# Kernel optimization log

Measured on AMD Instinct MI355X. Metric: run time of the kernel, lower is better.

## Reference

```python
import jax, jax.numpy as jnp
import numpy as np

B, N, D, H, K, R = 128, 2048, 256, 16, 32, 16
LEAKY_SLOPE = 0.01


def setup_inputs() -> dict:
    key = jax.random.key(0)
    ks = jax.random.split(key, 8)
    s = 0.05
    inp = jax.random.normal(ks[0], (B * N, D), dtype=jnp.float32)
    batch_ids = jnp.repeat(jnp.arange(B, dtype=jnp.int32), N)  # equal-size graphs
    Wk = jax.random.normal(ks[1], (K, D), dtype=jnp.float32) * s
    Wq0 = jax.random.normal(ks[2], (H * K, D), dtype=jnp.float32) * s
    Wq1 = jax.random.normal(ks[3], (H * K, D), dtype=jnp.float32) * s
    We = jax.random.normal(ks[4], (R, D), dtype=jnp.float32) * s
    Wout = jax.random.normal(ks[5], (D, H * R), dtype=jnp.float32) * s
    bout = jax.random.normal(ks[6], (D,), dtype=jnp.float32) * s
    return {"inp": inp, "batch_ids": batch_ids, "Wk": Wk, "Wq0": Wq0,
            "Wq1": Wq1, "We": We, "Wout": Wout, "bout": bout}


def reference(inp, batch_ids, Wk, Wq0, Wq1, We, Wout, bout):
    b = int(jnp.max(batch_ids)) + 1  # number of graphs (static at trace time)
    d = inp.shape[-1]
    # global max pool per graph (torch_geometric global_max_pool)
    pooled = jax.ops.segment_max(inp, batch_ids, num_segments=b)  # [B, D]
    x = inp.reshape(b, -1, d)                                     # [B, N, D]
    keys = jnp.einsum('bnd,kd->bnk', x, Wk)                       # [B, N, K]

    def head_embed(Wq):
        q = (pooled @ Wq.T).reshape(b, H, K)                      # [B, H, K]
        logits = jnp.einsum('bhk,bnk->bhn', q, keys)              # [B, H, N]
        att = jax.nn.softmax(logits, axis=-1)
        feat = jnp.einsum('bhn,bnd->bhd', att, x)                 # [B, H, D]
        return jnp.einsum('bhd,rd->bhr', feat, We)                # [B, H, R]

    dx = (head_embed(Wq0) - head_embed(Wq1)).reshape(b, -1)       # [B, H*R]
    out = dx @ Wout.T + bout
    return jnp.where(out >= 0, out, LEAKY_SLOPE * out)            # LeakyReLU
```

## Files before the change

### kernel.cpp

```cpp
#include <hip/hip_runtime.h>
#include <math.h>

#define B_ 128
#define N_ 2048
#define D_ 256
#define NHEADS 32

#define POOLED_OFF 0
#define PHI_OFF    32768
#define PLO_OFF    557056
#define ML_OFF     1081344
#define FEATP_OFF  1114112
#define XHI_OFF    5308416
#define XLO_OFF    38862848

#define XHI_S 0
#define XLO_S 32768
#define ATT_S 0
#define XT_S  33280
#define STAT_S 53760

typedef __attribute__((ext_vector_type(8))) short short8;
typedef __attribute__((ext_vector_type(4))) float f32x4;

__device__ __forceinline__ void atomic_max_f32(float* addr, float v) {
    if (v >= 0.0f) atomicMax((int*)addr, __float_as_int(v + 0.0f));
    else           atomicMin((unsigned int*)addr, __float_as_uint(v));
}
__device__ __forceinline__ unsigned short f2bf(float f) {
    unsigned u = __float_as_uint(f);
    u += 0x7fff + ((u >> 16) & 1);
    return (unsigned short)(u >> 16);
}
__device__ __forceinline__ float bf2f(unsigned short h) {
    return __uint_as_float(((unsigned)h) << 16);
}
__device__ __forceinline__ unsigned pack2bf(float a, float b) {
    return (unsigned)f2bf(a) | ((unsigned)f2bf(b) << 16);
}

__global__ __launch_bounds__(256) void k_init(float* __restrict__ pooled) {
    pooled[blockIdx.x * 256 + threadIdx.x] = -INFINITY;
}

__global__ __launch_bounds__(256) void k_pool(const float* __restrict__ inp,
                                              float* __restrict__ pooled,
                                              unsigned short* __restrict__ xhi,
                                              unsigned short* __restrict__ xlo) {
    int b = blockIdx.x >> 4;
    int ch = blockIdx.x & 15;
    int t = threadIdx.x;
    int sub = t >> 6;
    int dq = (t & 63) * 4;
    const float* p = inp + ((size_t)(b * N_ + ch * 128 + sub)) * D_ + dq;
    size_t nodebase = (size_t)b * N_ + ch * 128 + sub;
    float4 m = {-INFINITY, -INFINITY, -INFINITY, -INFINITY};
#pragma unroll 4
    for (int i = 0; i < 32; ++i) {
        float4 v = *(const float4*)(p + (size_t)i * 4 * D_);
        m.x = fmaxf(m.x, v.x); m.y = fmaxf(m.y, v.y);
        m.z = fmaxf(m.z, v.z); m.w = fmaxf(m.w, v.w);
        size_t node = nodebase + (size_t)i * 4;
        ushort4 h4, l4;
        h4.x = f2bf(v.x); l4.x = f2bf(v.x - bf2f(h4.x));
        h4.y = f2bf(v.y); l4.y = f2bf(v.y - bf2f(h4.y));
        h4.z = f2bf(v.z); l4.z = f2bf(v.z - bf2f(h4.z));
        h4.w = f2bf(v.w); l4.w = f2bf(v.w - bf2f(h4.w));
        *(ushort4*)(xhi + node * D_ + dq) = h4;
        *(ushort4*)(xlo + node * D_ + dq) = l4;
    }
    __shared__ float sm[4 * 256];
    sm[sub * 256 + dq + 0] = m.x;
    sm[sub * 256 + dq + 1] = m.y;
    sm[sub * 256 + dq + 2] = m.z;
    sm[sub * 256 + dq + 3] = m.w;
    __syncthreads();
    float v = fmaxf(fmaxf(sm[t], sm[256 + t]), fmaxf(sm[512 + t], sm[768 + t]));
    atomic_max_f32(pooled + b * D_ + t, v);
}

__global__ __launch_bounds__(256) void k_qp(const float* __restrict__ pooled,
                                            const float* __restrict__ Wq0,
                                            const float* __restrict__ Wq1,
                                            const float* __restrict__ Wk,
                                            unsigned short* __restrict__ Phi,
                                            unsigned short* __restrict__ Plo) {
    __shared__ float pl[D_];
    __shared__ float ql[1024];
    int b = blockIdx.x, t = threadIdx.x;
    pl[t] = pooled[b * D_ + t];
    __syncthreads();
    for (int rep = 0; rep < 4; ++rep) {
        int idx = rep * 256 + t;
        const float* Wq = (idx < 512) ? Wq0 : Wq1;
        int row = idx & 511;
        const float4* wr = (const float4*)(Wq + (size_t)row * D_);
        float acc = 0.0f;
        for (int dqi = 0; dqi < 64; ++dqi) {
            float4 w = wr[dqi];
            const float* pp = &pl[dqi * 4];
            acc += w.x * pp[0] + w.y * pp[1] + w.z * pp[2] + w.w * pp[3];
        }
        ql[idx] = acc;
    }
    __syncthreads();
    float wk[32];
#pragma unroll
    for (int k = 0; k < 32; ++k) wk[k] = Wk[k * D_ + t];
    for (int j = 0; j < NHEADS; ++j) {
        const float* q = &ql[(j >> 4) * 512 + (j & 15) * 32];
        float acc = 0.0f;
#pragma unroll
        for (int k = 0; k < 32; ++k) acc = fmaf(q[k], wk[k], acc);
        unsigned short hi = f2bf(acc);
        unsigned short lo = f2bf(acc - bf2f(hi));
        Phi[((size_t)b * NHEADS + j) * D_ + t] = hi;
        Plo[((size_t)b * NHEADS + j) * D_ + t] = lo;
    }
}

__global__ __launch_bounds__(256) void k_attn(const unsigned short* __restrict__ xhi,
                                              const unsigned short* __restrict__ xlo,
                                              const unsigned short* __restrict__ Phi,
                                              const unsigned short* __restrict__ Plo,
                                              float* __restrict__ ml,
                                              float* __restrict__ featp) {
    __shared__ uint4 smem4[4096];
    unsigned char* smem = (unsigned char*)smem4;
    float* smax = (float*)(smem + STAT_S);
    float* ssum = (float*)(smem + STAT_S + 512);

    int b = blockIdx.x >> 2, ns = blockIdx.x & 3;
    int t = threadIdx.x;
    int w = t >> 6;
    int lane = t & 63;
    int lq = lane >> 4;
    int lm = lane & 15;
    size_t gnode0 = (size_t)b * N_ + ns * 512;

    f32x4 acc_s[8][2];
#pragma unroll
    for (int mt = 0; mt < 8; ++mt)
#pragma unroll
        for (int ht = 0; ht < 2; ++ht) acc_s[mt][ht] = (f32x4){0.f, 0.f, 0.f, 0.f};

    int srow = t >> 2, sseg = t & 3;
    for (int dc = 0; dc < 8; ++dc) {
        int d0 = dc * 32;
        short8 bh[2], bl[2];
#pragma unroll
        for (int ht = 0; ht < 2; ++ht) {
            size_t poff = ((size_t)b * NHEADS + ht * 16 + lm) * D_ + d0 + lq * 8;
            bh[ht] = *(const short8*)(Phi + poff);
            bl[ht] = *(const short8*)(Plo + poff);
        }
        const unsigned short* gxh = xhi + (gnode0 + srow) * D_ + d0 + sseg * 8;
        const unsigned short* gxl = xlo + (gnode0 + srow) * D_ + d0 + sseg * 8;
        __syncthreads();
#pragma unroll
        for (int i = 0; i < 8; ++i) {
            *(uint4*)(smem + XHI_S + (size_t)(srow + i * 64) * 64 + sseg * 16) =
                *(const uint4*)(gxh + (size_t)i * 64 * D_);
            *(uint4*)(smem + XLO_S + (size_t)(srow + i * 64) * 64 + sseg * 16) =
                *(const uint4*)(gxl + (size_t)i * 64 * D_);
        }
        __syncthreads();
#pragma unroll
        for (int mt = 0; mt < 8; ++mt) {
            size_t roff = (size_t)(w * 128 + mt * 16 + lm) * 64 + lq * 16;
            short8 ah = *(const short8*)(smem + XHI_S + roff);
            short8 al = *(const short8*)(smem + XLO_S + roff);
#pragma unroll
            for (int ht = 0; ht < 2; ++ht) {
                acc_s[mt][ht] = __builtin_amdgcn_mfma_f32_16x16x32_bf16(ah, bh[ht], acc_s[mt][ht], 0, 0, 0);
                acc_s[mt][ht] = __builtin_amdgcn_mfma_f32_16x16x32_bf16(ah, bl[ht], acc_s[mt][ht], 0, 0, 0);
                acc_s[mt][ht] = __builtin_amdgcn_mfma_f32_16x16x32_bf16(al, bh[ht], acc_s[mt][ht], 0, 0, 0);
            }
        }
    }
    __syncthreads();

    float bm[2];
#pragma unroll
    for (int ht = 0; ht < 2; ++ht) {
        float m = -INFINITY;
#pragma unroll
        for (int mt = 0; mt < 8; ++mt) {
            m = fmaxf(m, fmaxf(fmaxf(acc_s[mt][ht][0], acc_s[mt][ht][1]),
                               fmaxf(acc_s[mt][ht][2], acc_s[mt][ht][3])));
        }
        m = fmaxf(m, __shfl_xor(m, 16));
        m = fmaxf(m, __shfl_xor(m, 32));
        if (lane < 16) smax[w * 32 + ht * 16 + lane] = m;
    }
    __syncthreads();
#pragma unroll
    for (int ht = 0; ht < 2; ++ht) {
        bm[ht] = fmaxf(fmaxf(smax[0 * 32 + ht * 16 + lm], smax[1 * 32 + ht * 16 + lm]),
                       fmaxf(smax[2 * 32 + ht * 16 + lm], smax[3 * 32 + ht * 16 + lm]));
    }
#pragma unroll
    for (int ht = 0; ht < 2; ++ht) {
        float s = 0.0f;
#pragma unroll
        for (int mt = 0; mt < 8; ++mt) {
            float e0 = __expf(acc_s[mt][ht][0] - bm[ht]);
            float e1 = __expf(acc_s[mt][ht][1] - bm[ht]);
            float e2 = __expf(acc_s[mt][ht][2] - bm[ht]);
            float e3 = __expf(acc_s[mt][ht][3] - bm[ht]);
            s += (e0 + e1) + (e2 + e3);
            uint2 pk;
            pk.x = pack2bf(e0, e1);
            pk.y = pack2bf(e2, e3);
            *(uint2*)(smem + ATT_S + (size_t)(ht * 16 + lm) * 1040 +
                      (size_t)(w * 128 + mt * 16 + lq * 4) * 2) = pk;
        }
        s += __shfl_xor(s, 16);
        s += __shfl_xor(s, 32);
        if (lane < 16) ssum[w * 32 + ht * 16 + lane] = s;
    }
    __syncthreads();
    if (t < 32) {
        float mB = fmaxf(fmaxf(smax[t], smax[32 + t]), fmaxf(smax[64 + t], smax[96 + t]));
        float l = ssum[t] + ssum[32 + t] + ssum[64 + t] + ssum[96 + t];
        float* mlp = ml + (((size_t)b * NHEADS + t) * 4 + ns) * 2;
        mlp[0] = mB;
        mlp[1] = l;
    }
    __syncthreads();

    f32x4 acc_o[2][4];
#pragma unroll
    for (int mt = 0; mt < 2; ++mt)
#pragma unroll
        for (int dt = 0; dt < 4; ++dt) acc_o[mt][dt] = (f32x4){0.f, 0.f, 0.f, 0.f};

    int db = t & 31, nb = t >> 5;
    for (int c = 0; c < 16; ++c) {
        const unsigned short* gx = xhi + (gnode0 + c * 32 + nb * 4) * D_ + db * 8;
        uint4 R0 = *(const uint4*)(gx);
        uint4 R1 = *(const uint4*)(gx + D_);
        uint4 R2 = *(const uint4*)(gx + 2 * D_);
        uint4 R3 = *(const uint4*)(gx + 3 * D_);
        const unsigned* r0 = (const unsigned*)&R0;
        const unsigned* r1 = (const unsigned*)&R1;
        const unsigned* r2 = (const unsigned*)&R2;
        const unsigned* r3 = (const unsigned*)&R3;
        uint2 T[8];
#pragma unroll
        for (int c2 = 0; c2 < 4; ++c2) {
            T[2 * c2 + 0].x = __builtin_amdgcn_perm(r1[c2], r0[c2], 0x05040100u);
            T[2 * c2 + 0].y = __builtin_amdgcn_perm(r3[c2], r2[c2], 0x05040100u);
            T[2 * c2 + 1].x = __builtin_amdgcn_perm(r1[c2], r0[c2], 0x07060302u);
            T[2 * c2 + 1].y = __builtin_amdgcn_perm(r3[c2], r2[c2], 0x07060302u);
        }
        __syncthreads();
#pragma unroll
        for (int j = 0; j < 8; ++j) {
            int jj = (j + db) & 7;
            *(uint2*)(smem + XT_S + (size_t)(db * 8 + jj) * 80 + nb * 8) = T[jj];
        }
        __syncthreads();
        short8 a0 = *(const short8*)(smem + ATT_S + (size_t)lm * 1040 + (size_t)(c * 32 + lq * 8) * 2);
        short8 a1 = *(const short8*)(smem + ATT_S + (size_t)(16 + lm) * 1040 + (size_t)(c * 32 + lq * 8) * 2);
#pragma unroll
        for (int dt = 0; dt < 4; ++dt) {
            short8 bf = *(const short8*)(smem + XT_S + (size_t)(w * 64 + dt * 16 + lm) * 80 + lq * 16);
            acc_o[0][dt] = __builtin_amdgcn_mfma_f32_16x16x32_bf16(a0, bf, acc_o[0][dt], 0, 0, 0);
            acc_o[1][dt] = __builtin_amdgcn_mfma_f32_16x16x32_bf16(a1, bf, acc_o[1][dt], 0, 0, 0);
        }
    }
    float* fb = featp + ((size_t)(ns * B_ + b)) * D_ * NHEADS;
#pragma unroll
    for (int mt = 0; mt < 2; ++mt)
#pragma unroll
        for (int dt = 0; dt < 4; ++dt) {
            int d = w * 64 + dt * 16 + lm;
            int h0 = mt * 16 + lq * 4;
            *(f32x4*)(fb + (size_t)d * NHEADS + h0) = acc_o[mt][dt];
        }
}

__global__ __launch_bounds__(256) void k_out(const float* __restrict__ featp,
                                             const float* __restrict__ ml,
                                             const float* __restrict__ We,
                                             const float* __restrict__ Wout,
                                             const float* __restrict__ bout,
                                             float* __restrict__ out) {
    __shared__ float f[NHEADS * 257];
    __shared__ float bhrs[512];
    __shared__ float dxs[256];
    __shared__ float wns[4 * 32];
    __shared__ float linv2[32];
    int b = blockIdx.x, t = threadIdx.x;
    if (t < 32) {
        const float* mlb = ml + ((size_t)b * NHEADS + t) * 8;
        float M = fmaxf(fmaxf(mlb[0], mlb[2]), fmaxf(mlb[4], mlb[6]));
        float e0 = __expf(mlb[0] - M), e1 = __expf(mlb[2] - M);
        float e2 = __expf(mlb[4] - M), e3 = __expf(mlb[6] - M);
        float L = e0 * mlb[1] + e1 * mlb[3] + e2 * mlb[5] + e3 * mlb[7];
        wns[0 * 32 + t] = e0; wns[1 * 32 + t] = e1;
        wns[2 * 32 + t] = e2; wns[3 * 32 + t] = e3;
        linv2[t] = 1.0f / L;
    }
    __syncthreads();
    float fj[32];
#pragma unroll
    for (int j = 0; j < 32; ++j) fj[j] = 0.0f;
#pragma unroll
    for (int ns = 0; ns < 4; ++ns) {
        const float* fp = featp + ((size_t)(ns * B_ + b) * D_ + t) * NHEADS;
#pragma unroll
        for (int j4 = 0; j4 < 8; ++j4) {
            float4 v = *(const float4*)(fp + j4 * 4);
            fj[j4 * 4 + 0] += wns[ns * 32 + j4 * 4 + 0] * v.x;
            fj[j4 * 4 + 1] += wns[ns * 32 + j4 * 4 + 1] * v.y;
            fj[j4 * 4 + 2] += wns[ns * 32 + j4 * 4 + 2] * v.z;
            fj[j4 * 4 + 3] += wns[ns * 32 + j4 * 4 + 3] * v.w;
        }
    }
#pragma unroll
    for (int j = 0; j < 32; ++j) f[j * 257 + t] = fj[j] * linv2[j];
    __syncthreads();
    for (int rep = 0; rep < 2; ++rep) {
        int idx = rep * 256 + t;
        int j = idx >> 4, r = idx & 15;
        const float* wrow = We + (size_t)r * D_;
        const float* ff = &f[j * 257];
        float acc = 0.0f;
        for (int d = 0; d < D_; ++d) acc = fmaf(ff[d], wrow[d], acc);
        bhrs[idx] = acc;
    }
    __syncthreads();
    {
        int h = t >> 4, r = t & 15;
        dxs[t] = bhrs[h * 16 + r] - bhrs[(16 + h) * 16 + r];
    }
    __syncthreads();
    float acc = bout[t];
    const float* wrow = Wout + (size_t)t * 256;
    for (int c = 0; c < 256; ++c) acc = fmaf(dxs[c], wrow[c], acc);
    out[(size_t)b * D_ + t] = acc >= 0.0f ? acc : 0.01f * acc;
}

extern "C" void kernel_launch(void* const* d_in, const int* in_sizes, int n_in,
                              void* d_out, int out_size, void* d_ws, size_t ws_size,
                              hipStream_t stream) {
    const float* inp  = (const float*)d_in[0];
    const float* Wk   = (const float*)d_in[2];
    const float* Wq0  = (const float*)d_in[3];
    const float* Wq1  = (const float*)d_in[4];
    const float* We   = (const float*)d_in[5];
    const float* Wout = (const float*)d_in[6];
    const float* bout = (const float*)d_in[7];
    float* out = (float*)d_out;
    float* ws  = (float*)d_ws;
    float* pooled = ws + POOLED_OFF;
    unsigned short* Phi = (unsigned short*)(ws + PHI_OFF);
    unsigned short* Plo = (unsigned short*)(ws + PLO_OFF);
    float* ml     = ws + ML_OFF;
    float* featp  = ws + FEATP_OFF;
    unsigned short* xhi = (unsigned short*)(ws + XHI_OFF);
    unsigned short* xlo = (unsigned short*)(ws + XLO_OFF);

    k_init<<<dim3(128), dim3(256), 0, stream>>>(pooled);
    k_pool<<<dim3(2048), dim3(256), 0, stream>>>(inp, pooled, xhi, xlo);
    k_qp<<<dim3(128), dim3(256), 0, stream>>>(pooled, Wq0, Wq1, Wk, Phi, Plo);
    k_attn<<<dim3(512), dim3(256), 0, stream>>>(xhi, xlo, Phi, Plo, ml, featp);
    k_out<<<dim3(128), dim3(256), 0, stream>>>(featp, ml, We, Wout, bout, out);
}
```

Measured before the change: 609.4 us.

## Fuse bf16 hi/lo split into attention kernel with online softmax over node chunks

The pooling kernel no longer writes bf16 hi/lo copies of the input. The attention kernel now reads fp32 input directly and converts to bf16 in registers. Attention is restructured into a single pass over 64-node chunks with a running max and sum (online softmax), fusing the score and weighted-sum phases. This removes the large intermediate write and re-read of x. In exchange, x is read from fp32 twice per chunk, there are extra barriers per chunk, and the hi split now truncates where it used to round, which changes numerics slightly.

Result: slower. 635.5 us (+4.3%).

```diff
diff --git a/kernel.cpp b/kernel.cpp
--- a/kernel.cpp
+++ b/kernel.cpp
@@ -11,18 +11,21 @@
 #define PLO_OFF    557056
 #define ML_OFF     1081344
 #define FEATP_OFF  1114112
-#define XHI_OFF    5308416
-#define XLO_OFF    38862848
-
-#define XHI_S 0
-#define XLO_S 32768
-#define ATT_S 0
-#define XT_S  33280
-#define STAT_S 53760
+
+#define XT_S    0
+#define ATT_S   36864
+#define SMAX_S  41472
+#define SSUM_S  41984
+#define ALPHA_S 42496
+#define MNEW_S  42624
+#define LDS_TOT 42752
 
 typedef __attribute__((ext_vector_type(8))) short short8;
 typedef __attribute__((ext_vector_type(4))) float f32x4;
 
+__device__ __forceinline__ unsigned perm(unsigned a, unsigned b, unsigned s) {
+    return __builtin_amdgcn_perm(a, b, s);
+}
 __device__ __forceinline__ void atomic_max_f32(float* addr, float v) {
     if (v >= 0.0f) atomicMax((int*)addr, __float_as_int(v + 0.0f));
     else           atomicMin((unsigned int*)addr, __float_as_uint(v));
@@ -38,36 +41,57 @@
 __device__ __forceinline__ unsigned pack2bf(float a, float b) {
     return (unsigned)f2bf(a) | ((unsigned)f2bf(b) << 16);
 }
+__device__ __forceinline__ short8 make_s8(unsigned a, unsigned b, unsigned c, unsigned d) {
+    union { unsigned u[4]; short8 s; } x;
+    x.u[0] = a; x.u[1] = b; x.u[2] = c; x.u[3] = d;
+    return x.s;
+}
+__device__ __forceinline__ void cvt_hilo(const float4& f0, const float4& f1,
+                                         short8& hi, short8& lo) {
+    unsigned u0 = __float_as_uint(f0.x), u1 = __float_as_uint(f0.y);
+    unsigned u2 = __float_as_uint(f0.z), u3 = __float_as_uint(f0.w);
+    unsigned u4 = __float_as_uint(f1.x), u5 = __float_as_uint(f1.y);
+    unsigned u6 = __float_as_uint(f1.z), u7 = __float_as_uint(f1.w);
+    hi = make_s8(perm(u1, u0, 0x07060302u), perm(u3, u2, 0x07060302u),
+                 perm(u5, u4, 0x07060302u), perm(u7, u6, 0x07060302u));
+    unsigned r0 = __float_as_uint(f0.x - __uint_as_float(u0 & 0xffff0000u));
+    unsigned r1 = __float_as_uint(f0.y - __uint_as_float(u1 & 0xffff0000u));
+    unsigned r2 = __float_as_uint(f0.z - __uint_as_float(u2 & 0xffff0000u));
+    unsigned r3 = __float_as_uint(f0.w - __uint_as_float(u3 & 0xffff0000u));
+    unsigned r4 = __float_as_uint(f1.x - __uint_as_float(u4 & 0xffff0000u));
+    unsigned r5 = __float_as_uint(f1.y - __uint_as_float(u5 & 0xffff0000u));
+    unsigned r6 = __float_as_uint(f1.z - __uint_as_float(u6 & 0xffff0000u));
+    unsigned r7 = __float_as_uint(f1.w - __uint_as_float(u7 & 0xffff0000u));
+    lo = make_s8(perm(r1, r0, 0x07060302u), perm(r3, r2, 0x07060302u),
+                 perm(r5, r4, 0x07060302u), perm(r7, r6, 0x07060302u));
+}
+__device__ __forceinline__ void packrow(const float4& a, const float4& b, unsigned w[4]) {
+    unsigned u0 = __float_as_uint(a.x) + 0x8000u, u1 = __float_as_uint(a.y) + 0x8000u;
+    unsigned u2 = __float_as_uint(a.z) + 0x8000u, u3 = __float_as_uint(a.w) + 0x8000u;
+    unsigned u4 = __float_as_uint(b.x) + 0x8000u, u5 = __float_as_uint(b.y) + 0x8000u;
+    unsigned u6 = __float_as_uint(b.z) + 0x8000u, u7 = __float_as_uint(b.w) + 0x8000u;
+    w[0] = perm(u1, u0, 0x07060302u); w[1] = perm(u3, u2, 0x07060302u);
+    w[2] = perm(u5, u4, 0x07060302u); w[3] = perm(u7, u6, 0x07060302u);
+}
 
 __global__ __launch_bounds__(256) void k_init(float* __restrict__ pooled) {
     pooled[blockIdx.x * 256 + threadIdx.x] = -INFINITY;
 }
 
 __global__ __launch_bounds__(256) void k_pool(const float* __restrict__ inp,
-                                              float* __restrict__ pooled,
-                                              unsigned short* __restrict__ xhi,
-                                              unsigned short* __restrict__ xlo) {
+                                              float* __restrict__ pooled) {
     int b = blockIdx.x >> 4;
     int ch = blockIdx.x & 15;
     int t = threadIdx.x;
     int sub = t >> 6;
     int dq = (t & 63) * 4;
     const float* p = inp + ((size_t)(b * N_ + ch * 128 + sub)) * D_ + dq;
-    size_t nodebase = (size_t)b * N_ + ch * 128 + sub;
     float4 m = {-INFINITY, -INFINITY, -INFINITY, -INFINITY};
-#pragma unroll 4
+#pragma unroll 8
     for (int i = 0; i < 32; ++i) {
         float4 v = *(const float4*)(p + (size_t)i * 4 * D_);
         m.x = fmaxf(m.x, v.x); m.y = fmaxf(m.y, v.y);
         m.z = fmaxf(m.z, v.z); m.w = fmaxf(m.w, v.w);
-        size_t node = nodebase + (size_t)i * 4;
-        ushort4 h4, l4;
-        h4.x = f2bf(v.x); l4.x = f2bf(v.x - bf2f(h4.x));
-        h4.y = f2bf(v.y); l4.y = f2bf(v.y - bf2f(h4.y));
-        h4.z = f2bf(v.z); l4.z = f2bf(v.z - bf2f(h4.z));
-        h4.w = f2bf(v.w); l4.w = f2bf(v.w - bf2f(h4.w));
-        *(ushort4*)(xhi + node * D_ + dq) = h4;
-        *(ushort4*)(xlo + node * D_ + dq) = l4;
     }
     __shared__ float sm[4 * 256];
     sm[sub * 256 + dq + 0] = m.x;
@@ -119,166 +143,161 @@
     }
 }
 
-__global__ __launch_bounds__(256) void k_attn(const unsigned short* __restrict__ xhi,
-                                              const unsigned short* __restrict__ xlo,
+__global__ __launch_bounds__(256) void k_attn(const float* __restrict__ inp,
                                               const unsigned short* __restrict__ Phi,
                                               const unsigned short* __restrict__ Plo,
                                               float* __restrict__ ml,
                                               float* __restrict__ featp) {
-    __shared__ uint4 smem4[4096];
-    unsigned char* smem = (unsigned char*)smem4;
-    float* smax = (float*)(smem + STAT_S);
-    float* ssum = (float*)(smem + STAT_S + 512);
+    __shared__ uint4 smem4[LDS_TOT / 16];
+    char* smem = (char*)smem4;
+    float* smax   = (float*)(smem + SMAX_S);
+    float* ssum   = (float*)(smem + SSUM_S);
+    float* alphas = (float*)(smem + ALPHA_S);
+    float* mnews  = (float*)(smem + MNEW_S);
 
     int b = blockIdx.x >> 2, ns = blockIdx.x & 3;
     int t = threadIdx.x;
-    int w = t >> 6;
-    int lane = t & 63;
-    int lq = lane >> 4;
-    int lm = lane & 15;
+    int w = t >> 6, lane = t & 63, lq = lane >> 4, lm = lane & 15;
     size_t gnode0 = (size_t)b * N_ + ns * 512;
 
-    f32x4 acc_s[8][2];
-#pragma unroll
-    for (int mt = 0; mt < 8; ++mt)
-#pragma unroll
-        for (int ht = 0; ht < 2; ++ht) acc_s[mt][ht] = (f32x4){0.f, 0.f, 0.f, 0.f};
-
-    int srow = t >> 2, sseg = t & 3;
-    for (int dc = 0; dc < 8; ++dc) {
-        int d0 = dc * 32;
-        short8 bh[2], bl[2];
-#pragma unroll
-        for (int ht = 0; ht < 2; ++ht) {
-            size_t poff = ((size_t)b * NHEADS + ht * 16 + lm) * D_ + d0 + lq * 8;
-            bh[ht] = *(const short8*)(Phi + poff);
-            bl[ht] = *(const short8*)(Plo + poff);
-        }
-        const unsigned short* gxh = xhi + (gnode0 + srow) * D_ + d0 + sseg * 8;
-        const unsigned short* gxl = xlo + (gnode0 + srow) * D_ + d0 + sseg * 8;
+    float Mrun = -INFINITY, lrun = 0.0f;
+    f32x4 acc_o[2][4];
+#pragma unroll
+    for (int ht = 0; ht < 2; ++ht)
+#pragma unroll
+        for (int dt = 0; dt < 4; ++dt) acc_o[ht][dt] = (f32x4){0.f, 0.f, 0.f, 0.f};
+
+    for (int cc = 0; cc < 8; ++cc) {
         __syncthreads();
 #pragma unroll
-        for (int i = 0; i < 8; ++i) {
-            *(uint4*)(smem + XHI_S + (size_t)(srow + i * 64) * 64 + sseg * 16) =
-                *(const uint4*)(gxh + (size_t)i * 64 * D_);
-            *(uint4*)(smem + XLO_S + (size_t)(srow + i * 64) * 64 + sseg * 16) =
-                *(const uint4*)(gxl + (size_t)i * 64 * D_);
-        }
+        for (int rep = 0; rep < 2; ++rep) {
+            int id = t + 256 * rep;
+            int sn = id & 15, sd = id >> 4;
+            const float* gp = inp + (gnode0 + cc * 64 + sn * 4) * (size_t)D_ + sd * 8;
+            unsigned w0[4], w1[4], w2[4], w3[4];
+            {
+                float4 a = *(const float4*)(gp), bq = *(const float4*)(gp + 4);
+                packrow(a, bq, w0);
+            }
+            {
+                float4 a = *(const float4*)(gp + D_), bq = *(const float4*)(gp + D_ + 4);
+                packrow(a, bq, w1);
+            }
+            {
+                float4 a = *(const float4*)(gp + 2 * D_), bq = *(const float4*)(gp + 2 * D_ + 4);
+                packrow(a, bq, w2);
+            }
+            {
+                float4 a = *(const float4*)(gp + 3 * D_), bq = *(const float4*)(gp + 3 * D_ + 4);
+                packrow(a, bq, w3);
+            }
+            uint2 T[8];
+#pragma unroll
+            for (int c2 = 0; c2 < 4; ++c2) {
+                T[2 * c2 + 0].x = perm(w1[c2], w0[c2], 0x05040100u);
+                T[2 * c2 + 0].y = perm(w3[c2], w2[c2], 0x05040100u);
+                T[2 * c2 + 1].x = perm(w1[c2], w0[c2], 0x07060302u);
+                T[2 * c2 + 1].y = perm(w3[c2], w2[c2], 0x07060302u);
+            }
+#pragma unroll
+            for (int j = 0; j < 8; ++j) {
+                int jj = (j + sd) & 7;
+                *(uint2*)(smem + XT_S + (size_t)(sd * 8 + jj) * 144 + sn * 8) = T[jj];
+            }
+        }
+        f32x4 acc_s[2];
+        acc_s[0] = (f32x4){0.f, 0.f, 0.f, 0.f};
+        acc_s[1] = (f32x4){0.f, 0.f, 0.f, 0.f};
+        const float* xr = inp + (gnode0 + cc * 64 + w * 16 + lm) * (size_t)D_ + lq * 8;
+#pragma unroll
+        for (int dc = 0; dc < 8; ++dc) {
+            float4 f0 = *(const float4*)(xr + dc * 32);
+            float4 f1 = *(const float4*)(xr + dc * 32 + 4);
+            short8 ah, al;
+            cvt_hilo(f0, f1, ah, al);
+#pragma unroll
+            for (int ht = 0; ht < 2; ++ht) {
+                size_t poff = ((size_t)b * NHEADS + ht * 16 + lm) * D_ + dc * 32 + lq * 8;
+                short8 bh = *(const short8*)(Phi + poff);
+                short8 bl = *(const short8*)(Plo + poff);
+                acc_s[ht] = __builtin_amdgcn_mfma_f32_16x16x32_bf16(ah, bh, acc_s[ht], 0, 0, 0);
+                acc_s[ht] = __builtin_amdgcn_mfma_f32_16x16x32_bf16(ah, bl, acc_s[ht], 0, 0, 0);
+                acc_s[ht] = __builtin_amdgcn_mfma_f32_16x16x32_bf16(al, bh, acc_s[ht], 0, 0, 0);
+            }
+        }
+        float m0 = fmaxf(fmaxf(acc_s[0][0], acc_s[0][1]), fmaxf(acc_s[0][2], acc_s[0][3]));
+        float m1 = fmaxf(fmaxf(acc_s[1][0], acc_s[1][1]), fmaxf(acc_s[1][2], acc_s[1][3]));
+        m0 = fmaxf(m0, __shfl_xor(m0, 16)); m0 = fmaxf(m0, __shfl_xor(m0, 32));
+        m1 = fmaxf(m1, __shfl_xor(m1, 16)); m1 = fmaxf(m1, __shfl_xor(m1, 32));
+        if (lane < 32) smax[w * 32 + lane] = (lane < 16) ? m0 : m1;
         __syncthreads();
-#pragma unroll
-        for (int mt = 0; mt < 8; ++mt) {
-            size_t roff = (size_t)(w * 128 + mt * 16 + lm) * 64 + lq * 16;
-            short8 ah = *(const short8*)(smem + XHI_S + roff);
-            short8 al = *(const short8*)(smem + XLO_S + roff);
-#pragma unroll
-            for (int ht = 0; ht < 2; ++ht) {
-                acc_s[mt][ht] = __builtin_amdgcn_mfma_f32_16x16x32_bf16(ah, bh[ht], acc_s[mt][ht], 0, 0, 0);
-                acc_s[mt][ht] = __builtin_amdgcn_mfma_f32_16x16x32_bf16(ah, bl[ht], acc_s[mt][ht], 0, 0, 0);
-                acc_s[mt][ht] = __builtin_amdgcn_mfma_f32_16x16x32_bf16(al, bh[ht], acc_s[mt][ht], 0, 0, 0);
-            }
-        }
-    }
-    __syncthreads();
-
-    float bm[2];
-#pragma unroll
-    for (int ht = 0; ht < 2; ++ht) {
-        float m = -INFINITY;
-#pragma unroll
-        for (int mt = 0; mt < 8; ++mt) {
-            m = fmaxf(m, fmaxf(fmaxf(acc_s[mt][ht][0], acc_s[mt][ht][1]),
-                               fmaxf(acc_s[mt][ht][2], acc_s[mt][ht][3])));
-        }
-        m = fmaxf(m, __shfl_xor(m, 16));
-        m = fmaxf(m, __shfl_xor(m, 32));
-        if (lane < 16) smax[w * 32 + ht * 16 + lane] = m;
-    }
-    __syncthreads();
-#pragma unroll
-    for (int ht = 0; ht < 2; ++ht) {
-        bm[ht] = fmaxf(fmaxf(smax[0 * 32 + ht * 16 + lm], smax[1 * 32 + ht * 16 + lm]),
-                       fmaxf(smax[2 * 32 + ht * 16 + lm], smax[3 * 32 + ht * 16 + lm]));
-    }
-#pragma unroll
-    for (int ht = 0; ht < 2; ++ht) {
-        float s = 0.0f;
-#pragma unroll
-        for (int mt = 0; mt < 8; ++mt) {
-            float e0 = __expf(acc_s[mt][ht][0] - bm[ht]);
-            float e1 = __expf(acc_s[mt][ht][1] - bm[ht]);
-            float e2 = __expf(acc_s[mt][ht][2] - bm[ht]);
-            float e3 = __expf(acc_s[mt][ht][3] - bm[ht]);
-            s += (e0 + e1) + (e2 + e3);
-            uint2 pk;
-            pk.x = pack2bf(e0, e1);
-            pk.y = pack2bf(e2, e3);
-            *(uint2*)(smem + ATT_S + (size_t)(ht * 16 + lm) * 1040 +
-                      (size_t)(w * 128 + mt * 16 + lq * 4) * 2) = pk;
-        }
-        s += __shfl_xor(s, 16);
-        s += __shfl_xor(s, 32);
-        if (lane < 16) ssum[w * 32 + ht * 16 + lane] = s;
-    }
-    __syncthreads();
-    if (t < 32) {
-        float mB = fmaxf(fmaxf(smax[t], smax[32 + t]), fmaxf(smax[64 + t], smax[96 + t]));
-        float l = ssum[t] + ssum[32 + t] + ssum[64 + t] + ssum[96 + t];
-        float* mlp = ml + (((size_t)b * NHEADS + t) * 4 + ns) * 2;
-        mlp[0] = mB;
-        mlp[1] = l;
-    }
-    __syncthreads();
-
-    f32x4 acc_o[2][4];
-#pragma unroll
-    for (int mt = 0; mt < 2; ++mt)
-#pragma unroll
-        for (int dt = 0; dt < 4; ++dt) acc_o[mt][dt] = (f32x4){0.f, 0.f, 0.f, 0.f};
-
-    int db = t & 31, nb = t >> 5;
-    for (int c = 0; c < 16; ++c) {
-        const unsigned short* gx = xhi + (gnode0 + c * 32 + nb * 4) * D_ + db * 8;
-        uint4 R0 = *(const uint4*)(gx);
-        uint4 R1 = *(const uint4*)(gx + D_);
-        uint4 R2 = *(const uint4*)(gx + 2 * D_);
-        uint4 R3 = *(const uint4*)(gx + 3 * D_);
-        const unsigned* r0 = (const unsigned*)&R0;
-        const unsigned* r1 = (const unsigned*)&R1;
-        const unsigned* r2 = (const unsigned*)&R2;
-        const unsigned* r3 = (const unsigned*)&R3;
-        uint2 T[8];
-#pragma unroll
-        for (int c2 = 0; c2 < 4; ++c2) {
-            T[2 * c2 + 0].x = __builtin_amdgcn_perm(r1[c2], r0[c2], 0x05040100u);
-            T[2 * c2 + 0].y = __builtin_amdgcn_perm(r3[c2], r2[c2], 0x05040100u);
-            T[2 * c2 + 1].x = __builtin_amdgcn_perm(r1[c2], r0[c2], 0x07060302u);
-            T[2 * c2 + 1].y = __builtin_amdgcn_perm(r3[c2], r2[c2], 0x07060302u);
+        float alpha_r = 0.0f;
+        if (t < 32) {
+            float mc = fmaxf(fmaxf(smax[t], smax[32 + t]), fmaxf(smax[64 + t], smax[96 + t]));
+            float Mn = fmaxf(Mrun, mc);
+            alpha_r = __expf(Mrun - Mn);
+            Mrun = Mn;
+            alphas[t] = alpha_r;
+            mnews[t] = Mn;
         }
         __syncthreads();
-#pragma unroll
-        for (int j = 0; j < 8; ++j) {
-            int jj = (j + db) & 7;
-            *(uint2*)(smem + XT_S + (size_t)(db * 8 + jj) * 80 + nb * 8) = T[jj];
+        float Mn0 = mnews[lm], Mn1 = mnews[16 + lm];
+        {
+            float e0 = __expf(acc_s[0][0] - Mn0), e1 = __expf(acc_s[0][1] - Mn0);
+            float e2 = __expf(acc_s[0][2] - Mn0), e3 = __expf(acc_s[0][3] - Mn0);
+            float s0 = (e0 + e1) + (e2 + e3);
+            uint2 pk; pk.x = pack2bf(e0, e1); pk.y = pack2bf(e2, e3);
+            *(uint2*)(smem + ATT_S + (size_t)lm * 144 + (w * 16 + lq * 4) * 2) = pk;
+            float f0 = __expf(acc_s[1][0] - Mn1), f1 = __expf(acc_s[1][1] - Mn1);
+            float f2 = __expf(acc_s[1][2] - Mn1), f3 = __expf(acc_s[1][3] - Mn1);
+            float s1 = (f0 + f1) + (f2 + f3);
+            pk.x = pack2bf(f0, f1); pk.y = pack2bf(f2, f3);
+            *(uint2*)(smem + ATT_S + (size_t)(16 + lm) * 144 + (w * 16 + lq * 4) * 2) = pk;
+            s0 += __shfl_xor(s0, 16); s0 += __shfl_xor(s0, 32);
+            s1 += __shfl_xor(s1, 16); s1 += __shfl_xor(s1, 32);
+            if (lane < 32) ssum[w * 32 + lane] = (lane < 16) ? s0 : s1;
+        }
+        float4 al0 = *(const float4*)(alphas + lq * 4);
+        float4 al1 = *(const float4*)(alphas + 16 + lq * 4);
+#pragma unroll
+        for (int dt = 0; dt < 4; ++dt) {
+            acc_o[0][dt][0] *= al0.x; acc_o[0][dt][1] *= al0.y;
+            acc_o[0][dt][2] *= al0.z; acc_o[0][dt][3] *= al0.w;
+            acc_o[1][dt][0] *= al1.x; acc_o[1][dt][1] *= al1.y;
+            acc_o[1][dt][2] *= al1.z; acc_o[1][dt][3] *= al1.w;
         }
         __syncthreads();
-        short8 a0 = *(const short8*)(smem + ATT_S + (size_t)lm * 1040 + (size_t)(c * 32 + lq * 8) * 2);
-        short8 a1 = *(const short8*)(smem + ATT_S + (size_t)(16 + lm) * 1040 + (size_t)(c * 32 + lq * 8) * 2);
-#pragma unroll
-        for (int dt = 0; dt < 4; ++dt) {
-            short8 bf = *(const short8*)(smem + XT_S + (size_t)(w * 64 + dt * 16 + lm) * 80 + lq * 16);
-            acc_o[0][dt] = __builtin_amdgcn_mfma_f32_16x16x32_bf16(a0, bf, acc_o[0][dt], 0, 0, 0);
-            acc_o[1][dt] = __builtin_amdgcn_mfma_f32_16x16x32_bf16(a1, bf, acc_o[1][dt], 0, 0, 0);
-        }
-    }
-    float* fb = featp + ((size_t)(ns * B_ + b)) * D_ * NHEADS;
-#pragma unroll
-    for (int mt = 0; mt < 2; ++mt)
+        if (t < 32) {
+            float s4 = ssum[t] + ssum[32 + t] + ssum[64 + t] + ssum[96 + t];
+            lrun = lrun * alpha_r + s4;
+        }
+#pragma unroll
+        for (int ks = 0; ks < 2; ++ks) {
+            short8 a0 = *(const short8*)(smem + ATT_S + (size_t)lm * 144 + ks * 64 + lq * 16);
+            short8 a1 = *(const short8*)(smem + ATT_S + (size_t)(16 + lm) * 144 + ks * 64 + lq * 16);
+#pragma unroll
+            for (int dt = 0; dt < 4; ++dt) {
+                short8 bf = *(const short8*)(smem + XT_S +
+                             (size_t)(w * 64 + dt * 16 + lm) * 144 + ks * 64 + lq * 16);
+                acc_o[0][dt] = __builtin_amdgcn_mfma_f32_16x16x32_bf16(a0, bf, acc_o[0][dt], 0, 0, 0);
+                acc_o[1][dt] = __builtin_amdgcn_mfma_f32_16x16x32_bf16(a1, bf, acc_o[1][dt], 0, 0, 0);
+            }
+        }
+    }
+    float* fb = featp + (size_t)(ns * B_ + b) * D_ * NHEADS;
+#pragma unroll
+    for (int ht = 0; ht < 2; ++ht)
 #pragma unroll
         for (int dt = 0; dt < 4; ++dt) {
             int d = w * 64 + dt * 16 + lm;
-            int h0 = mt * 16 + lq * 4;
-            *(f32x4*)(fb + (size_t)d * NHEADS + h0) = acc_o[mt][dt];
-        }
+            int h0 = ht * 16 + lq * 4;
+            *(f32x4*)(fb + (size_t)d * NHEADS + h0) = acc_o[ht][dt];
+        }
+    if (t < 32) {
+        float* mlp = ml + (((size_t)b * NHEADS + t) * 4 + ns) * 2;
+        mlp[0] = Mrun;
+        mlp[1] = lrun;
+    }
 }
 
 __global__ __launch_bounds__(256) void k_out(const float* __restrict__ featp,
@@ -360,12 +379,10 @@
     unsigned short* Plo = (unsigned short*)(ws + PLO_OFF);
     float* ml     = ws + ML_OFF;
     float* featp  = ws + FEATP_OFF;
-    unsigned short* xhi = (unsigned short*)(ws + XHI_OFF);
-    unsigned short* xlo = (unsigned short*)(ws + XLO_OFF);
 
     k_init<<<dim3(128), dim3(256), 0, stream>>>(pooled);
-    k_pool<<<dim3(2048), dim3(256), 0, stream>>>(inp, pooled, xhi, xlo);
+    k_pool<<<dim3(2048), dim3(256), 0, stream>>>(inp, pooled);
     k_qp<<<dim3(128), dim3(256), 0, stream>>>(pooled, Wq0, Wq1, Wk, Phi, Plo);
-    k_attn<<<dim3(512), dim3(256), 0, stream>>>(xhi, xlo, Phi, Plo, ml, featp);
+    k_attn<<<dim3(512), dim3(256), 0, stream>>>(inp, Phi, Plo, ml, featp);
     k_out<<<dim3(128), dim3(256), 0, stream>>>(featp, ml, We, Wout, bout, out);
 }
```
